# Kernel tuning notes

Measured on AMD Instinct MI355X. Metric: run time of the kernel, lower is better.

The kernel has to match this reference:

```python
import jax, jax.numpy as jnp
from jax import lax
import numpy as np

D_MODEL = 128
N_HEADS = 8
N_POINTS = 8
MAX_MAG = 10.0
NEG_SLOPE = 0.1


def conv2d(x, w, b, pad):
    # x: (N, Cin, H, W), w: (Cout, Cin, kh, kw)
    y = lax.conv_general_dilated(x, w, (1, 1), [(pad, pad), (pad, pad)],
                                 dimension_numbers=('NCHW', 'OIHW', 'NCHW'))
    return y + b[None, :, None, None]


def leaky(x):
    return jnp.where(x >= 0, x, NEG_SLOPE * x)


def bilinear_sample(img, grid):
    # img: (B, C, H, W); grid: (B, P, H, W, 2) in [-1, 1] (x, y)
    # Matches torch F.grid_sample(mode='bilinear', padding_mode='zeros', align_corners=False)
    B, C, H, W = img.shape
    x = ((grid[..., 0] + 1.0) * W - 1.0) * 0.5
    y = ((grid[..., 1] + 1.0) * H - 1.0) * 0.5
    x0 = jnp.floor(x)
    y0 = jnp.floor(y)
    wx1 = x - x0
    wy1 = y - y0

    def one(img_b, x0b, y0b, wx1b, wy1b):
        def gather(xi, yi):
            valid = (xi >= 0) & (xi < W) & (yi >= 0) & (yi < H)
            xc = jnp.clip(xi, 0, W - 1).astype(jnp.int32)
            yc = jnp.clip(yi, 0, H - 1).astype(jnp.int32)
            v = img_b[:, yc, xc]  # (C, P, H, W)
            return v * valid
        wx0b = 1.0 - wx1b
        wy0b = 1.0 - wy1b
        v00 = gather(x0b, y0b)
        v01 = gather(x0b + 1, y0b)
        v10 = gather(x0b, y0b + 1)
        v11 = gather(x0b + 1, y0b + 1)
        return (v00 * (wx0b * wy0b) + v01 * (wx1b * wy0b)
                + v10 * (wx0b * wy1b) + v11 * (wx1b * wy1b))

    return jax.vmap(one)(img, x0, y0, wx1, wy1)  # (B, C, P, H, W)


def ss_deform_attn(value, loc):
    # value: (N, nh, d, H, W); loc: (N, nh, P, H, W, 2) in normalized [0,1] coords
    N, nh, d, H, W = value.shape
    P = loc.shape[2]
    v = value.reshape(N * nh, d, H, W)
    grids = (2.0 * loc - 1.0).reshape(N * nh, P, H, W, 2)
    sampled = bilinear_sample(v, grids)  # (N*nh, d, P, H, W)
    # per-location attention logits = <sampled_point, value_at_location>
    scores = jnp.einsum('ndphw,ndhw->nphw', sampled, v)
    aw = jax.nn.softmax(scores, axis=1)
    out = jnp.einsum('ndphw,nphw->ndhw', sampled, aw)
    return out.reshape(N, nh * d, H, W)


def _forward(query, value, reference_points, co_w1, co_b1, co_w2, co_b2,
             co_w3, co_b3, co_w4, co_b4, val_w, val_b, out_w, out_b):
    N, C, H, W = value.shape
    v = conv2d(value, val_w, val_b, 0)
    v = v.reshape(N, N_HEADS, D_MODEL // N_HEADS, H, W)
    o = leaky(conv2d(query, co_w1, co_b1, 1))
    o = leaky(conv2d(o, co_w2, co_b2, 1))
    o = leaky(conv2d(o, co_w3, co_b3, 1))
    o = conv2d(o, co_w4, co_b4, 1)
    o = MAX_MAG * jnp.tanh(o)
    offsets = o.reshape(N, N_HEADS, N_POINTS, H, W, 2)
    norm = jnp.array([W, H], dtype=o.dtype)  # (x, y) normalizer
    loc = reference_points[:, None, None, :, :, :] + offsets / norm
    out = ss_deform_attn(v, loc)
    return conv2d(out, out_w, out_b, 0)


def setup_inputs() -> dict:
    key = jax.random.key(0)
    ks = jax.random.split(key, 12)
    N, H, W = 4, 80, 80

    def w_init(k, shape):
        fan_in = shape[1] * shape[2] * shape[3]
        return jax.random.normal(k, shape, jnp.float32) / np.sqrt(fan_in)

    return {
        'query': jax.random.normal(ks[0], (N, 2 * D_MODEL, H, W), jnp.float32),
        'value': jax.random.normal(ks[1], (N, D_MODEL, H, W), jnp.float32),
        'reference_points': jax.random.uniform(ks[2], (N, H, W, 2), jnp.float32),
        'co_w1': w_init(ks[3], (D_MODEL, 2 * D_MODEL, 3, 3)),
        'co_b1': jnp.zeros((D_MODEL,), jnp.float32),
        'co_w2': w_init(ks[4], (D_MODEL, D_MODEL, 3, 3)),
        'co_b2': jnp.zeros((D_MODEL,), jnp.float32),
        'co_w3': w_init(ks[5], (D_MODEL, D_MODEL, 3, 3)),
        'co_b3': jnp.zeros((D_MODEL,), jnp.float32),
        'co_w4': w_init(ks[6], (N_HEADS * N_POINTS * 2, D_MODEL, 3, 3)),
        'co_b4': jnp.zeros((N_HEADS * N_POINTS * 2,), jnp.float32),
        'val_w': w_init(ks[7], (D_MODEL, D_MODEL, 1, 1)),
        'val_b': jnp.zeros((D_MODEL,), jnp.float32),
        'out_w': w_init(ks[8], (D_MODEL, D_MODEL, 1, 1)),
        'out_b': jnp.zeros((D_MODEL,), jnp.float32),
    }


def reference(query, value, reference_points, co_w1, co_b1, co_w2, co_b2,
              co_w3, co_b3, co_w4, co_b4, val_w, val_b, out_w, out_b):
    return _forward(query, value, reference_points, co_w1, co_b1, co_w2, co_b2,
                    co_w3, co_b3, co_w4, co_b4, val_w, val_b, out_w, out_b)
```

## Files before the change

### kernel.cpp

```cpp
#include <hip/hip_runtime.h>
#include <math.h>

#define Hh 80
#define Ww 80
#define HW 6400
#define PS 6724
#define NB 4

typedef _Float16 half8 __attribute__((ext_vector_type(8)));
typedef _Float16 half4v __attribute__((ext_vector_type(4)));
typedef float f32x16 __attribute__((ext_vector_type(16)));

__device__ __forceinline__ void gload16(const _Float16* g, _Float16* l) {
    __builtin_amdgcn_global_load_lds(
        (const __attribute__((address_space(1))) void*)g,
        (__attribute__((address_space(3))) void*)l, 16, 0, 0);
}

#define WAITVM(N) asm volatile("s_waitcnt vmcnt(" #N ")" ::: "memory")
#define FENCE() asm volatile("" ::: "memory")

__device__ __forceinline__ void barrier_mem() {
    asm volatile("" ::: "memory");
    __builtin_amdgcn_s_barrier();
    asm volatile("" ::: "memory");
}

__device__ inline void wblob_one(const float* src, _Float16* dst, int CI, int d) {
    int NC = CI / 32;
    int j = d & 7;
    int l = (d >> 3) & 63;
    int h = (d >> 9) & 1;
    int rest = d >> 10;
    int tap = rest % 9;
    rest /= 9;
    int c = rest % NC;
    int CT = rest / NC;
    int co = CT * 32 + (l & 31);
    int ci = c * 32 + h * 16 + (l >> 5) * 8 + j;
    dst[d] = (_Float16)src[((size_t)co * CI + ci) * 9 + tap];
}

__device__ inline void wblob1x1_one(const float* src, _Float16* dst, int d) {
    int j = d & 7;
    int l = (d >> 3) & 63;
    int c = (d >> 9) & 7;
    int CT = d >> 12;
    int co = CT * 32 + (l & 31);
    int ci = c * 16 + (l >> 5) * 8 + j;
    dst[d] = (_Float16)src[co * 128 + ci];
}

__device__ inline int padsite(int p) {
    if (p < 82) return p;
    if (p < 164) return 81 * 82 + (p - 82);
    if (p < 244) return (p - 163) * 82;
    return (p - 243) * 82 + 81;
}

__global__ __launch_bounds__(256) void prep_all(
    const float* __restrict__ w1, const float* __restrict__ w2,
    const float* __restrict__ w3, const float* __restrict__ w4,
    const float* __restrict__ vw, const float* __restrict__ ow,
    _Float16* __restrict__ b1, _Float16* __restrict__ b2,
    _Float16* __restrict__ b3, _Float16* __restrict__ b4,
    _Float16* __restrict__ bv, _Float16* __restrict__ bo,
    int* __restrict__ qh_i, int* __restrict__ hA_i, int* __restrict__ hB_i,
    const float* __restrict__ query, const float* __restrict__ value,
    _Float16* __restrict__ q_h, _Float16* __restrict__ v_h) {
    __shared__ _Float16 T[64 * 264];
    const int blk = blockIdx.x;
    const int t = threadIdx.x;

    if (blk < 4304) {
        int idx = blk * 256 + t;
        if (idx < 294912) { wblob_one(w1, b1, 256, idx); return; }
        idx -= 294912;
        if (idx < 147456) { wblob_one(w2, b2, 128, idx); return; }
        idx -= 147456;
        if (idx < 147456) { wblob_one(w3, b3, 128, idx); return; }
        idx -= 147456;
        if (idx < 147456) { wblob_one(w4, b4, 128, idx); return; }
        idx -= 147456;
        if (idx < 16384) { wblob1x1_one(vw, bv, idx); return; }
        idx -= 16384;
        if (idx < 16384) { wblob1x1_one(ow, bo, idx); return; }
        idx -= 16384;
        if (idx < 165888) {
            int n = idx / 41472, rr = idx % 41472;
            int c = rr / 5184, r2 = rr % 5184;
            int p = r2 >> 4, k = r2 & 15;
            qh_i[((size_t)(n * 8 + c) * PS + padsite(p)) * 16 + k] = 0;
            return;
        }
        idx -= 165888;
        if (idx < 82944) {
            int n = idx / 20736, rr = idx % 20736;
            int c = rr / 5184, r2 = rr % 5184;
            int p = r2 >> 4, k = r2 & 15;
            hA_i[((size_t)(n * 4 + c) * PS + padsite(p)) * 16 + k] = 0;
            return;
        }
        idx -= 82944;
        if (idx < 82944) {
            int n = idx / 20736, rr = idx % 20736;
            int c = rr / 5184, r2 = rr % 5184;
            int p = r2 >> 4, k = r2 & 15;
            hB_i[((size_t)(n * 4 + c) * PS + padsite(p)) * 16 + k] = 0;
        }
        return;
    }

    if (blk < 4704) {
        const int b = blk - 4304;
        const int xcd = b & 7, n = xcd & 3, hi = xcd >> 2;
        const int s0 = hi * 3200 + (b >> 3) * 64;
        constexpr int CI = 256, ST = CI + 8;
        for (int idx = t; idx < 64 * CI; idx += 256) {
            int ci = idx >> 6, sl = idx & 63;
            T[sl * ST + ci] = (_Float16)query[((size_t)n * CI + ci) * HW + s0 + sl];
        }
        __syncthreads();
        for (int idx = t; idx < 64 * 32; idx += 256) {
            int q = idx & 31, sl = idx >> 5;
            int s = s0 + sl, yy = s / 80, xx = s % 80;
            int c = q >> 2, off = (q & 3) * 8;
            *(int4*)(q_h + ((size_t)(n * 8 + c) * PS + (yy + 1) * 82 + (xx + 1)) * 32 + off) =
                *(const int4*)(&T[sl * ST + q * 8]);
        }
        return;
    }

    {
        const int b = blk - 4704;
        const int xcd = b & 7, n = xcd & 3, hi = xcd >> 2;
        const int s0 = hi * 3200 + (b >> 3) * 64;
        constexpr int CI = 128, ST = CI + 8;
        for (int idx = t; idx < 64 * CI; idx += 256) {
            int ci = idx >> 6, sl = idx & 63;
            T[sl * ST + ci] = (_Float16)value[((size_t)n * CI + ci) * HW + s0 + sl];
        }
        __syncthreads();
        for (int idx = t; idx < 64 * 16; idx += 256) {
            int q = idx & 15, sl = idx >> 4;
            *(int4*)(v_h + ((size_t)n * HW + s0 + sl) * CI + q * 8) =
                *(const int4*)(&T[sl * ST + q * 8]);
        }
    }
}

template <int NCp, int ACT>
__global__ __launch_bounds__(256, 2) void conv3x3_mfma(
    const _Float16* __restrict__ in, const _Float16* __restrict__ wblob,
    const float* __restrict__ bias, void* __restrict__ outp) {
    constexpr int NS = NCp * 18;
    static_assert((NCp & 1) == 0, "pair loop needs even NCp");
    __shared__ _Float16 Bbuf[2][6 * 1024];

    const int b = blockIdx.x;
    const int xcd = b & 7, n = xcd & 3, hi = xcd >> 2;
    const int r = b >> 3;
    const int x0 = (r % 5) * 16, y0 = hi * 40 + (r / 5) * 4;
    const int t = threadIdx.x;
    const int w = t >> 6, l = t & 63;
    const int lane31 = l & 31, lhalf = l >> 5;
    const int lx = lane31 & 15, lyw = lane31 >> 4;
    const int si = l & 15, g8 = l >> 4;

    const _Float16* bplane0 = in + (size_t)(n * NCp) * PS * 32;
    const _Float16* wA = wblob + (size_t)w * NS * 512 + l * 8;

    f32x16 acc0 = {}, acc1 = {};
    half8 aA[6], aB[6];

    auto stageB = [&](const _Float16* plane, int par) {
#pragma unroll
        for (int j = 0; j < 3; ++j) {
            const int m = 3 * w + j, rr = m >> 1, sg = m & 1;
            gload16(plane + ((size_t)((y0 + rr) * 82 + x0 + sg * 16 + si)) * 32 + g8 * 8,
                    &Bbuf[par][rr * 1024 + sg * 512]);
        }
    };
    auto loadA6 = [&](half8 (&ar)[6], int grp) {
        const _Float16* asrc = wA + (size_t)grp * 6 * 512;
#pragma unroll
        for (int k2 = 0; k2 < 6; ++k2)
            ar[k2] = *(const half8*)(asrc + (size_t)k2 * 512);
    };
    auto compute6 = [&](int gi, const half8 (&ar)[6], const _Float16* bb) {
#pragma unroll
        for (int k = 0; k < 6; ++k) {
            const int u = gi * 6 + k;
            const int tap = u >> 1, h = u & 1;
            const int dy = tap / 3, dx = tap % 3;
            const int cx = lx + dx;
            const int boff = (cx >> 4) * 512 + (h * 2 + lhalf) * 128 + (cx & 15) * 8;
            half8 b0 = *(const half8*)&bb[(lyw + dy) * 1024 + boff];
            half8 b1 = *(const half8*)&bb[(lyw + 2 + dy) * 1024 + boff];
            acc0 = __builtin_amdgcn_mfma_f32_32x32x16_f16(ar[k], b0, acc0, 0, 0, 0);
            acc1 = __builtin_amdgcn_mfma_f32_32x32x16_f16(ar[k], b1, acc1, 0, 0, 0);
        }
    };

    stageB(bplane0, 0);
    loadA6(aA, 0);
    WAITVM(0);
    barrier_mem();

#pragma unroll 1
    for (int cp = 0; cp < NCp / 2; ++cp) {
        const int c0 = 2 * cp;
        const bool lastp = (cp == NCp / 2 - 1);
        const _Float16* plane1 = bplane0 + (size_t)(c0 + 1) * PS * 32;
        const _Float16* plane2 = bplane0 + (size_t)(c0 + 2) * PS * 32;
        loadA6(aB, c0 * 3 + 1);
        stageB(plane1, 1);
        FENCE();
        compute6(0, aA, Bbuf[0]);
        loadA6(aA, c0 * 3 + 2);
        FENCE();
        compute6(1, aB, Bbuf[0]);
        loadA6(aB, c0 * 3 + 3);
        FENCE();
        compute6(2, aA, Bbuf[0]);
        WAITVM(12);
        barrier_mem();
        loadA6(aA, c0 * 3 + 4);
        if (!lastp) stageB(plane2, 0);
        FENCE();
        compute6(0, aB, Bbuf[1]);
        loadA6(aB, c0 * 3 + 5);
        FENCE();
        compute6(1, aA, Bbuf[1]);
        if (!lastp) {
            loadA6(aA, c0 * 3 + 6);
            FENCE();
            compute6(2, aB, Bbuf[1]);
            WAITVM(12);
            barrier_mem();
        } else {
            FENCE();
            compute6(2, aB, Bbuf[1]);
        }
    }

    const int x = x0 + lx;
#pragma unroll
    for (int f = 0; f < 2; ++f) {
        const f32x16& acc = f ? acc1 : acc0;
        const int y = y0 + lyw + 2 * f;
#pragma unroll
        for (int q = 0; q < 4; ++q) {
            const int inner = 8 * q + 4 * lhalf;
            const int co0 = w * 32 + inner;
            float v[4];
#pragma unroll
            for (int i = 0; i < 4; ++i) {
                float vv = acc[q * 4 + i] + bias[co0 + i];
                if (ACT == 1) vv = (vv >= 0.f) ? vv : 0.1f * vv;
                else vv = 10.f * tanhf(vv);
                v[i] = vv;
            }
            if (ACT == 1) {
                half4v hv = {(_Float16)v[0], (_Float16)v[1], (_Float16)v[2], (_Float16)v[3]};
                *(half4v*)((_Float16*)outp +
                    ((size_t)(n * 4 + w) * PS + (y + 1) * 82 + (x + 1)) * 32 + inner) = hv;
            } else {
                float4 fv = {v[0], v[1], v[2], v[3]};
                *(float4*)((float*)outp + ((size_t)n * HW + y * 80 + x) * 128 + co0) = fv;
            }
        }
    }
}

template <int MODE>
__global__ __launch_bounds__(256) void conv1x1_mfma(
    const _Float16* __restrict__ in, const _Float16* __restrict__ wblob,
    const float* __restrict__ bias, float* __restrict__ outp) {
    const int b = blockIdx.x;
    const int xcd = b & 7, n = xcd & 3, hi = xcd >> 2;
    const int r = b >> 3;
    const int coH = r & 1, strip = r >> 1;
    const int t = threadIdx.x;
    const int w = t >> 6, l = t & 63;
    const int lane31 = l & 31, lhalf = l >> 5;
    const int s = hi * 3200 + strip * 128 + w * 32 + lane31;

    const _Float16* pB = in + (size_t)(n * HW + s) * 128 + lhalf * 8;
    const _Float16* pA0 = wblob + (size_t)(coH * 2) * 8 * 512 + l * 8;
    const _Float16* pA1 = pA0 + 8 * 512;

    half8 bB[8], bA0[8], bA1[8];
#pragma unroll
    for (int c = 0; c < 8; ++c) {
        bB[c]  = *(const half8*)(pB + c * 16);
        bA0[c] = *(const half8*)(pA0 + (size_t)c * 512);
        bA1[c] = *(const half8*)(pA1 + (size_t)c * 512);
    }
    f32x16 acc0 = {}, acc1 = {};
#pragma unroll
    for (int c = 0; c < 8; ++c) {
        acc0 = __builtin_amdgcn_mfma_f32_32x32x16_f16(bA0[c], bB[c], acc0, 0, 0, 0);
        acc1 = __builtin_amdgcn_mfma_f32_32x32x16_f16(bA1[c], bB[c], acc1, 0, 0, 0);
    }

#pragma unroll
    for (int ct = 0; ct < 2; ++ct) {
        const f32x16& acc = ct ? acc1 : acc0;
#pragma unroll
        for (int q = 0; q < 4; ++q) {
            const int co0 = coH * 64 + ct * 32 + 8 * q + 4 * lhalf;
            if (MODE == 0) {
                const int hd = co0 >> 4, dd = co0 & 15;
                float4 fv = {acc[4 * q + 0] + bias[co0 + 0], acc[4 * q + 1] + bias[co0 + 1],
                             acc[4 * q + 2] + bias[co0 + 2], acc[4 * q + 3] + bias[co0 + 3]};
                *(float4*)&outp[((size_t)(n * 8 + hd) * HW + s) * 16 + dd] = fv;
            } else {
#pragma unroll
                for (int i = 0; i < 4; ++i)
                    outp[(size_t)(n * 128 + co0 + i) * HW + s] = acc[4 * q + i] + bias[co0 + i];
            }
        }
    }
}

__global__ __launch_bounds__(256, 2) void deform_attn_kernel(
    const float* __restrict__ v_s, const float* __restrict__ offs,
    const float* __restrict__ ref, _Float16* __restrict__ att) {
    const int slice = blockIdx.x;
    const int n = slice >> 3, hd = slice & 7;
    const int t = threadIdx.x;
    const int s = blockIdx.y * 64 + (t >> 2);
    const int d0 = (t & 3) * 4;
    const int nb = n * 8 + hd;
    const float* vbase = v_s + (size_t)nb * (HW * 16) + d0;

    const float4 cv = *(const float4*)&v_s[((size_t)nb * HW + s) * 16 + d0];
    const float rx = ref[(size_t)(n * HW + s) * 2 + 0] * 80.f - 0.5f;
    const float ry = ref[(size_t)(n * HW + s) * 2 + 1] * 80.f - 0.5f;

    const int e = (s >= 3200) ? 1 : 0;
    const float* ob0 = offs + ((size_t)n * HW + (2 * s - e * HW)) * 128 + hd * 16 + e;

    float4 oxv[4], oyv[4];
#pragma unroll
    for (int i = 0; i < 4; ++i) {
        oxv[i] = *(const float4*)(ob0 + i * 4);
        oyv[i] = *(const float4*)(ob0 + 128 + i * 4);
    }
    float ox[8], oy[8];
#pragma unroll
    for (int i = 0; i < 4; ++i) {
        ox[2 * i] = oxv[i].x; ox[2 * i + 1] = oxv[i].z;
        oy[2 * i] = oyv[i].x; oy[2 * i + 1] = oyv[i].z;
    }

    float wx1[8], wy1[8];
    int ix[8], iy[8];
#pragma unroll
    for (int p = 0; p < 8; ++p) {
        const float px = rx + ox[p];
        const float py = ry + oy[p];
        const float fx = floorf(px), fy = floorf(py);
        ix[p] = (int)fx; iy[p] = (int)fy;
        wx1[p] = px - fx; wy1[p] = py - fy;
    }

    float4 g[8][4];
#pragma unroll
    for (int p = 0; p < 8; ++p) {
        const int xc0 = min(max(ix[p], 0), 79),     xc1 = min(max(ix[p] + 1, 0), 79);
        const int yc0 = min(max(iy[p], 0), 79),     yc1 = min(max(iy[p] + 1, 0), 79);
        const int r0 = yc0 * 80, r1 = yc1 * 80;
        g[p][0] = *(const float4*)(vbase + (size_t)(r0 + xc0) * 16);
        g[p][1] = *(const float4*)(vbase + (size_t)(r0 + xc1) * 16);
        g[p][2] = *(const float4*)(vbase + (size_t)(r1 + xc0) * 16);
        g[p][3] = *(const float4*)(vbase + (size_t)(r1 + xc1) * 16);
    }

    float4 sampled[8];
    float score[8];
#pragma unroll
    for (int p = 0; p < 8; ++p) {
        const float vx0 = (ix[p] >= 0 && ix[p] < Ww) ? 1.f : 0.f;
        const float vx1 = (ix[p] + 1 >= 0 && ix[p] + 1 < Ww) ? 1.f : 0.f;
        const float vy0 = (iy[p] >= 0 && iy[p] < Hh) ? 1.f : 0.f;
        const float vy1 = (iy[p] + 1 >= 0 && iy[p] + 1 < Hh) ? 1.f : 0.f;
        const float wx0 = 1.f - wx1[p], wy0 = 1.f - wy1[p];
        const float w00 = wx0 * wy0 * vx0 * vy0;
        const float w01 = wx1[p] * wy0 * vx1 * vy0;
        const float w10 = wx0 * wy1[p] * vx0 * vy1;
        const float w11 = wx1[p] * wy1[p] * vx1 * vy1;
        float4 sv;
        sv.x = g[p][0].x * w00 + g[p][1].x * w01 + g[p][2].x * w10 + g[p][3].x * w11;
        sv.y = g[p][0].y * w00 + g[p][1].y * w01 + g[p][2].y * w10 + g[p][3].y * w11;
        sv.z = g[p][0].z * w00 + g[p][1].z * w01 + g[p][2].z * w10 + g[p][3].z * w11;
        sv.w = g[p][0].w * w00 + g[p][1].w * w01 + g[p][2].w * w10 + g[p][3].w * w11;
        sampled[p] = sv;
        float sc = sv.x * cv.x + sv.y * cv.y + sv.z * cv.z + sv.w * cv.w;
        sc += __shfl_xor(sc, 1);
        sc += __shfl_xor(sc, 2);
        score[p] = sc;
    }

    float m = score[0];
#pragma unroll
    for (int p = 1; p < 8; ++p) m = fmaxf(m, score[p]);
    float sum = 0.f, aw[8];
#pragma unroll
    for (int p = 0; p < 8; ++p) {
        aw[p] = __expf(score[p] - m);
        sum += aw[p];
    }
    const float inv = 1.f / sum;
    float4 o = {0.f, 0.f, 0.f, 0.f};
#pragma unroll
    for (int p = 0; p < 8; ++p) {
        o.x += aw[p] * sampled[p].x;
        o.y += aw[p] * sampled[p].y;
        o.z += aw[p] * sampled[p].z;
        o.w += aw[p] * sampled[p].w;
    }
    o.x *= inv; o.y *= inv; o.z *= inv; o.w *= inv;

    half4v hv = {(_Float16)o.x, (_Float16)o.y, (_Float16)o.z, (_Float16)o.w};
    *(half4v*)&att[((size_t)n * HW + s) * 128 + hd * 16 + d0] = hv;
}

extern "C" void kernel_launch(void* const* d_in, const int* in_sizes, int n_in,
                              void* d_out, int out_size, void* d_ws, size_t ws_size,
                              hipStream_t stream) {
    const float* query = (const float*)d_in[0];
    const float* value = (const float*)d_in[1];
    const float* ref   = (const float*)d_in[2];
    const float* co_w1 = (const float*)d_in[3];
    const float* co_b1 = (const float*)d_in[4];
    const float* co_w2 = (const float*)d_in[5];
    const float* co_b2 = (const float*)d_in[6];
    const float* co_w3 = (const float*)d_in[7];
    const float* co_b3 = (const float*)d_in[8];
    const float* co_w4 = (const float*)d_in[9];
    const float* co_b4 = (const float*)d_in[10];
    const float* val_w = (const float*)d_in[11];
    const float* val_b = (const float*)d_in[12];
    const float* out_w = (const float*)d_in[13];
    const float* out_b = (const float*)d_in[14];

    char* ws = (char*)d_ws;
    size_t o = 0;
    auto alloc = [&](size_t bytes) { char* p = ws + o; o += (bytes + 255) & ~(size_t)255; return p; };

    _Float16* wb2 = (_Float16*)alloc(147456 * 2);
    _Float16* wb3 = (_Float16*)alloc(147456 * 2);
    _Float16* wb4 = (_Float16*)alloc(147456 * 2);
    _Float16* wbv = (_Float16*)alloc(16384 * 2);
    _Float16* wbo = (_Float16*)alloc(16384 * 2);
    char* vsR = alloc(3276800 * 4);
    float* v_s = (float*)vsR;
    _Float16* wb1 = (_Float16*)vsR;
    _Float16* v_h = (_Float16*)alloc((size_t)NB * HW * 128 * 2);
    char* R1 = alloc((size_t)NB * 8 * PS * 32 * 2);
    _Float16* q_h = (_Float16*)R1;
    float* o4 = (float*)R1;
    char* R2 = alloc((size_t)NB * 4 * PS * 32 * 2 * 2);
    _Float16* hA = (_Float16*)R2;
    _Float16* hB = (_Float16*)(R2 + (size_t)NB * 4 * PS * 32 * 2);
    _Float16* att_h = (_Float16*)R2;

    prep_all<<<5104, 256, 0, stream>>>(co_w1, co_w2, co_w3, co_w4, val_w, out_w,
                                       wb1, wb2, wb3, wb4, wbv, wbo,
                                       (int*)q_h, (int*)hA, (int*)hB,
                                       query, value, q_h, v_h);

    conv3x3_mfma<8, 1><<<400, 256, 0, stream>>>(q_h, wb1, co_b1, hA);

    conv1x1_mfma<0><<<400, 256, 0, stream>>>(v_h, wbv, val_b, v_s);

    conv3x3_mfma<4, 1><<<400, 256, 0, stream>>>(hA, wb2, co_b2, hB);
    conv3x3_mfma<4, 1><<<400, 256, 0, stream>>>(hB, wb3, co_b3, hA);
    conv3x3_mfma<4, 2><<<400, 256, 0, stream>>>(hA, wb4, co_b4, o4);

    deform_attn_kernel<<<dim3(32, 100), 256, 0, stream>>>(v_s, o4, ref, att_h);

    conv1x1_mfma<1><<<400, 256, 0, stream>>>(att_h, wbo, out_b, (float*)d_out);
}
```

Before: 223.1 us.

## Stream deform-attn samples with online softmax and double-buffered gathers

The deform attention kernel no longer keeps all 32 gathered float4 values and the 8 sampled vectors in registers. It now prefetches the four corners for the next point while combining the current one, and folds the results into an online softmax accumulator. The launch bound goes from 2 to 4 blocks per SM to raise occupancy on the smaller register footprint. The cost is less memory-level parallelism per thread, since only two points' gathers are in flight at once, plus extra exp work for the rescaling.

```diff
diff --git a/kernel.cpp b/kernel.cpp
--- a/kernel.cpp
+++ b/kernel.cpp
@@ -324,7 +324,7 @@
     }
 }
 
-__global__ __launch_bounds__(256, 2) void deform_attn_kernel(
+__global__ __launch_bounds__(256, 4) void deform_attn_kernel(
     const float* __restrict__ v_s, const float* __restrict__ offs,
     const float* __restrict__ ref, _Float16* __restrict__ att) {
     const int slice = blockIdx.x;
@@ -355,72 +355,73 @@
         oy[2 * i] = oyv[i].x; oy[2 * i + 1] = oyv[i].z;
     }
 
-    float wx1[8], wy1[8];
-    int ix[8], iy[8];
-#pragma unroll
-    for (int p = 0; p < 8; ++p) {
+    auto coords = [&](int p, int& ix, int& iy, float& wx, float& wy) {
         const float px = rx + ox[p];
         const float py = ry + oy[p];
         const float fx = floorf(px), fy = floorf(py);
-        ix[p] = (int)fx; iy[p] = (int)fy;
-        wx1[p] = px - fx; wy1[p] = py - fy;
-    }
-
-    float4 g[8][4];
+        ix = (int)fx; iy = (int)fy;
+        wx = px - fx; wy = py - fy;
+    };
+    auto issue4 = [&](int ix, int iy, float4 (&g)[4]) {
+        const int xc0 = min(max(ix, 0), 79),     xc1 = min(max(ix + 1, 0), 79);
+        const int yc0 = min(max(iy, 0), 79),     yc1 = min(max(iy + 1, 0), 79);
+        const int r0 = yc0 * 80, r1 = yc1 * 80;
+        g[0] = *(const float4*)(vbase + (size_t)(r0 + xc0) * 16);
+        g[1] = *(const float4*)(vbase + (size_t)(r0 + xc1) * 16);
+        g[2] = *(const float4*)(vbase + (size_t)(r1 + xc0) * 16);
+        g[3] = *(const float4*)(vbase + (size_t)(r1 + xc1) * 16);
+    };
+    auto combine = [&](int ix, int iy, float wx1, float wy1,
+                       const float4 (&g)[4], float4& sv) {
+        const float vx0 = (ix >= 0 && ix < Ww) ? 1.f : 0.f;
+        const float vx1 = (ix + 1 >= 0 && ix + 1 < Ww) ? 1.f : 0.f;
+        const float vy0 = (iy >= 0 && iy < Hh) ? 1.f : 0.f;
+        const float vy1 = (iy + 1 >= 0 && iy + 1 < Hh) ? 1.f : 0.f;
+        const float wx0 = 1.f - wx1, wy0 = 1.f - wy1;
+        const float w00 = wx0 * wy0 * vx0 * vy0;
+        const float w01 = wx1 * wy0 * vx1 * vy0;
+        const float w10 = wx0 * wy1 * vx0 * vy1;
+        const float w11 = wx1 * wy1 * vx1 * vy1;
+        sv.x = g[0].x * w00 + g[1].x * w01 + g[2].x * w10 + g[3].x * w11;
+        sv.y = g[0].y * w00 + g[1].y * w01 + g[2].y * w10 + g[3].y * w11;
+        sv.z = g[0].z * w00 + g[1].z * w01 + g[2].z * w10 + g[3].z * w11;
+        sv.w = g[0].w * w00 + g[1].w * w01 + g[2].w * w10 + g[3].w * w11;
+    };
+
+    float4 gA[4], gB[4];
+    int ixA, iyA, ixB, iyB;
+    float wxA, wyA, wxB, wyB;
+
+    coords(0, ixA, iyA, wxA, wyA);
+    issue4(ixA, iyA, gA);
+
+    float m = -INFINITY, sum = 0.f;
+    float4 o = {0.f, 0.f, 0.f, 0.f};
+
 #pragma unroll
     for (int p = 0; p < 8; ++p) {
-        const int xc0 = min(max(ix[p], 0), 79),     xc1 = min(max(ix[p] + 1, 0), 79);
-        const int yc0 = min(max(iy[p], 0), 79),     yc1 = min(max(iy[p] + 1, 0), 79);
-        const int r0 = yc0 * 80, r1 = yc1 * 80;
-        g[p][0] = *(const float4*)(vbase + (size_t)(r0 + xc0) * 16);
-        g[p][1] = *(const float4*)(vbase + (size_t)(r0 + xc1) * 16);
-        g[p][2] = *(const float4*)(vbase + (size_t)(r1 + xc0) * 16);
-        g[p][3] = *(const float4*)(vbase + (size_t)(r1 + xc1) * 16);
-    }
-
-    float4 sampled[8];
-    float score[8];
-#pragma unroll
-    for (int p = 0; p < 8; ++p) {
-        const float vx0 = (ix[p] >= 0 && ix[p] < Ww) ? 1.f : 0.f;
-        const float vx1 = (ix[p] + 1 >= 0 && ix[p] + 1 < Ww) ? 1.f : 0.f;
-        const float vy0 = (iy[p] >= 0 && iy[p] < Hh) ? 1.f : 0.f;
-        const float vy1 = (iy[p] + 1 >= 0 && iy[p] + 1 < Hh) ? 1.f : 0.f;
-        const float wx0 = 1.f - wx1[p], wy0 = 1.f - wy1[p];
-        const float w00 = wx0 * wy0 * vx0 * vy0;
-        const float w01 = wx1[p] * wy0 * vx1 * vy0;
-        const float w10 = wx0 * wy1[p] * vx0 * vy1;
-        const float w11 = wx1[p] * wy1[p] * vx1 * vy1;
+        if (p + 1 < 8) {
+            if (p & 1) { coords(p + 1, ixA, iyA, wxA, wyA); issue4(ixA, iyA, gA); }
+            else       { coords(p + 1, ixB, iyB, wxB, wyB); issue4(ixB, iyB, gB); }
+        }
         float4 sv;
-        sv.x = g[p][0].x * w00 + g[p][1].x * w01 + g[p][2].x * w10 + g[p][3].x * w11;
-        sv.y = g[p][0].y * w00 + g[p][1].y * w01 + g[p][2].y * w10 + g[p][3].y * w11;
-        sv.z = g[p][0].z * w00 + g[p][1].z * w01 + g[p][2].z * w10 + g[p][3].z * w11;
-        sv.w = g[p][0].w * w00 + g[p][1].w * w01 + g[p][2].w * w10 + g[p][3].w * w11;
-        sampled[p] = sv;
+        if (p & 1) combine(ixB, iyB, wxB, wyB, gB, sv);
+        else       combine(ixA, iyA, wxA, wyA, gA, sv);
         float sc = sv.x * cv.x + sv.y * cv.y + sv.z * cv.z + sv.w * cv.w;
         sc += __shfl_xor(sc, 1);
         sc += __shfl_xor(sc, 2);
-        score[p] = sc;
-    }
-
-    float m = score[0];
-#pragma unroll
-    for (int p = 1; p < 8; ++p) m = fmaxf(m, score[p]);
-    float sum = 0.f, aw[8];
-#pragma unroll
-    for (int p = 0; p < 8; ++p) {
-        aw[p] = __expf(score[p] - m);
-        sum += aw[p];
-    }
+        const float mn = fmaxf(m, sc);
+        const float scale = __expf(m - mn);
+        const float ew = __expf(sc - mn);
+        sum = sum * scale + ew;
+        o.x = o.x * scale + ew * sv.x;
+        o.y = o.y * scale + ew * sv.y;
+        o.z = o.z * scale + ew * sv.z;
+        o.w = o.w * scale + ew * sv.w;
+        m = mn;
+    }
+
     const float inv = 1.f / sum;
-    float4 o = {0.f, 0.f, 0.f, 0.f};
-#pragma unroll
-    for (int p = 0; p < 8; ++p) {
-        o.x += aw[p] * sampled[p].x;
-        o.y += aw[p] * sampled[p].y;
-        o.z += aw[p] * sampled[p].z;
-        o.w += aw[p] * sampled[p].w;
-    }
     o.x *= inv; o.y *= inv; o.z *= inv; o.w *= inv;
 
     half4v hv = {(_Float16)o.x, (_Float16)o.y, (_Float16)o.z, (_Float16)o.w};
```

Result: no change. 226.8 us (+1.7%).

## Split deform-attention sampling points across thread pairs with online-softmax merge

Applied to the files above, without the earlier changes.

Each output location/channel-quad is now handled by two threads, each sampling four of the eight points, and the partial softmax results (max, sum, weighted accumulator) are merged via a cross-lane shuffle. This halves per-thread register pressure (gather buffers), so launch bounds move to four blocks per SM and the grid doubles, aiming to expose more memory-level parallelism for the gather-bound kernel. It adds extra shuffles and exp calls for the merge, and half the threads do no store.

```diff
diff --git a/kernel.cpp b/kernel.cpp
--- a/kernel.cpp
+++ b/kernel.cpp
@@ -324,14 +324,16 @@
     }
 }
 
-__global__ __launch_bounds__(256, 2) void deform_attn_kernel(
+__global__ __launch_bounds__(256, 4) void deform_attn_kernel(
     const float* __restrict__ v_s, const float* __restrict__ offs,
     const float* __restrict__ ref, _Float16* __restrict__ att) {
     const int slice = blockIdx.x;
     const int n = slice >> 3, hd = slice & 7;
     const int t = threadIdx.x;
-    const int s = blockIdx.y * 64 + (t >> 2);
-    const int d0 = (t & 3) * 4;
+    const int s = blockIdx.y * 32 + (t >> 3);
+    const int sub = t & 7;
+    const int d0 = (sub & 3) * 4;
+    const int ph = sub >> 2;
     const int nb = n * 8 + hd;
     const float* vbase = v_s + (size_t)nb * (HW * 16) + d0;
 
@@ -342,23 +344,17 @@
     const int e = (s >= 3200) ? 1 : 0;
     const float* ob0 = offs + ((size_t)n * HW + (2 * s - e * HW)) * 128 + hd * 16 + e;
 
-    float4 oxv[4], oyv[4];
-#pragma unroll
-    for (int i = 0; i < 4; ++i) {
-        oxv[i] = *(const float4*)(ob0 + i * 4);
-        oyv[i] = *(const float4*)(ob0 + 128 + i * 4);
-    }
-    float ox[8], oy[8];
-#pragma unroll
-    for (int i = 0; i < 4; ++i) {
-        ox[2 * i] = oxv[i].x; ox[2 * i + 1] = oxv[i].z;
-        oy[2 * i] = oyv[i].x; oy[2 * i + 1] = oyv[i].z;
-    }
-
-    float wx1[8], wy1[8];
-    int ix[8], iy[8];
-#pragma unroll
-    for (int p = 0; p < 8; ++p) {
+    float4 oxv0 = *(const float4*)(ob0 + 8 * ph);
+    float4 oxv1 = *(const float4*)(ob0 + 8 * ph + 4);
+    float4 oyv0 = *(const float4*)(ob0 + 128 + 8 * ph);
+    float4 oyv1 = *(const float4*)(ob0 + 128 + 8 * ph + 4);
+    float ox[4] = {oxv0.x, oxv0.z, oxv1.x, oxv1.z};
+    float oy[4] = {oyv0.x, oyv0.z, oyv1.x, oyv1.z};
+
+    float wx1[4], wy1[4];
+    int ix[4], iy[4];
+#pragma unroll
+    for (int p = 0; p < 4; ++p) {
         const float px = rx + ox[p];
         const float py = ry + oy[p];
         const float fx = floorf(px), fy = floorf(py);
@@ -366,9 +362,9 @@
         wx1[p] = px - fx; wy1[p] = py - fy;
     }
 
-    float4 g[8][4];
-#pragma unroll
-    for (int p = 0; p < 8; ++p) {
+    float4 g[4][4];
+#pragma unroll
+    for (int p = 0; p < 4; ++p) {
         const int xc0 = min(max(ix[p], 0), 79),     xc1 = min(max(ix[p] + 1, 0), 79);
         const int yc0 = min(max(iy[p], 0), 79),     yc1 = min(max(iy[p] + 1, 0), 79);
         const int r0 = yc0 * 80, r1 = yc1 * 80;
@@ -378,10 +374,10 @@
         g[p][3] = *(const float4*)(vbase + (size_t)(r1 + xc1) * 16);
     }
 
-    float4 sampled[8];
-    float score[8];
-#pragma unroll
-    for (int p = 0; p < 8; ++p) {
+    float4 sampled[4];
+    float score[4];
+#pragma unroll
+    for (int p = 0; p < 4; ++p) {
         const float vx0 = (ix[p] >= 0 && ix[p] < Ww) ? 1.f : 0.f;
         const float vx1 = (ix[p] + 1 >= 0 && ix[p] + 1 < Ww) ? 1.f : 0.f;
         const float vy0 = (iy[p] >= 0 && iy[p] < Hh) ? 1.f : 0.f;
@@ -405,26 +401,39 @@
 
     float m = score[0];
 #pragma unroll
-    for (int p = 1; p < 8; ++p) m = fmaxf(m, score[p]);
-    float sum = 0.f, aw[8];
-#pragma unroll
-    for (int p = 0; p < 8; ++p) {
-        aw[p] = __expf(score[p] - m);
-        sum += aw[p];
-    }
-    const float inv = 1.f / sum;
+    for (int p = 1; p < 4; ++p) m = fmaxf(m, score[p]);
+    float sum = 0.f;
     float4 o = {0.f, 0.f, 0.f, 0.f};
 #pragma unroll
-    for (int p = 0; p < 8; ++p) {
-        o.x += aw[p] * sampled[p].x;
-        o.y += aw[p] * sampled[p].y;
-        o.z += aw[p] * sampled[p].z;
-        o.w += aw[p] * sampled[p].w;
-    }
-    o.x *= inv; o.y *= inv; o.z *= inv; o.w *= inv;
-
-    half4v hv = {(_Float16)o.x, (_Float16)o.y, (_Float16)o.z, (_Float16)o.w};
-    *(half4v*)&att[((size_t)n * HW + s) * 128 + hd * 16 + d0] = hv;
+    for (int p = 0; p < 4; ++p) {
+        const float aw = __expf(score[p] - m);
+        sum += aw;
+        o.x += aw * sampled[p].x;
+        o.y += aw * sampled[p].y;
+        o.z += aw * sampled[p].z;
+        o.w += aw * sampled[p].w;
+    }
+
+    const float m2   = __shfl_xor(m, 4);
+    const float sum2 = __shfl_xor(sum, 4);
+    float4 o2;
+    o2.x = __shfl_xor(o.x, 4);
+    o2.y = __shfl_xor(o.y, 4);
+    o2.z = __shfl_xor(o.z, 4);
+    o2.w = __shfl_xor(o.w, 4);
+    const float mn = fmaxf(m, m2);
+    const float sA = __expf(m - mn), sB = __expf(m2 - mn);
+    const float tot = sum * sA + sum2 * sB;
+    const float inv = 1.f / tot;
+    o.x = (o.x * sA + o2.x * sB) * inv;
+    o.y = (o.y * sA + o2.y * sB) * inv;
+    o.z = (o.z * sA + o2.z * sB) * inv;
+    o.w = (o.w * sA + o2.w * sB) * inv;
+
+    if (ph == 0) {
+        half4v hv = {(_Float16)o.x, (_Float16)o.y, (_Float16)o.z, (_Float16)o.w};
+        *(half4v*)&att[((size_t)n * HW + s) * 128 + hd * 16 + d0] = hv;
+    }
 }
 
 extern "C" void kernel_launch(void* const* d_in, const int* in_sizes, int n_in,
@@ -480,7 +489,7 @@
     conv3x3_mfma<4, 1><<<400, 256, 0, stream>>>(hB, wb3, co_b3, hA);
     conv3x3_mfma<4, 2><<<400, 256, 0, stream>>>(hA, wb4, co_b4, o4);
 
-    deform_attn_kernel<<<dim3(32, 100), 256, 0, stream>>>(v_s, o4, ref, att_h);
+    deform_attn_kernel<<<dim3(32, 200), 256, 0, stream>>>(v_s, o4, ref, att_h);
 
     conv1x1_mfma<1><<<400, 256, 0, stream>>>(att_h, wbo, out_b, (float*)d_out);
 }
```

Result: no change. 219.2 us (-1.7%).
